# Optimization experiments

Measured on AMD Instinct MI355X. Metric: run time of the kernel, lower is better.

Reference implementation:

```python
import jax, jax.numpy as jnp
import numpy as np
from jax import lax

NUM_HEADS = 8  # init_kwargs: num_heads
TOPK = 7       # hard-coded in DMF.forward


def setup_inputs() -> dict:
    key = jax.random.key(0)
    k1, k2, k3, k4 = jax.random.split(key, 4)
    b, dim, H, W = 8, 384, 128, 128
    x = jax.random.normal(k1, (b, dim, H, W), dtype=jnp.float32)
    qkv_w = jax.random.normal(k2, (dim * 3, dim), dtype=jnp.float32) * 0.05   # 1x1 conv weight
    dw_w = jax.random.normal(k3, (dim * 3, 1, 3, 3), dtype=jnp.float32) * 0.05  # depthwise 3x3
    proj_w = jax.random.normal(k4, (dim, dim), dtype=jnp.float32) * 0.05     # 1x1 conv weight
    temperature = jnp.ones((NUM_HEADS, 1, 1), dtype=jnp.float32)
    return {"x": x, "qkv_w": qkv_w, "dw_w": dw_w, "proj_w": proj_w, "temperature": temperature}


def _l2norm(t, eps=1e-12):
    # matches torch.nn.functional.normalize(dim=-1)
    n = jnp.sqrt(jnp.sum(t * t, axis=-1, keepdims=True))
    return t / jnp.maximum(n, eps)


def reference(x, qkv_w, dw_w, proj_w, temperature):
    b, c, h, w = x.shape
    ch = c // NUM_HEADS  # channels per head

    # 1x1 conv (pointwise) -> depthwise 3x3 conv
    qkv = jnp.einsum('bchw,oc->bohw', x, qkv_w)
    qkv = lax.conv_general_dilated(
        qkv, dw_w, window_strides=(1, 1), padding=[(1, 1), (1, 1)],
        feature_group_count=qkv.shape[1],
        dimension_numbers=('NCHW', 'OIHW', 'NCHW'))
    q, k, v = jnp.split(qkv, 3, axis=1)

    def to_heads(t):  # b (head ch) h w -> b head ch (h w)
        return t.reshape(b, NUM_HEADS, ch, h * w)

    q = _l2norm(to_heads(q))
    k = _l2norm(to_heads(k))
    v = to_heads(v)

    # channel attention: [b, head, ch, ch]
    attn_weight = jnp.einsum('bhcn,bhdn->bhcd', q, k) * temperature

    # top-k sparsify along last dim, then masked softmax
    _, idx = lax.top_k(attn_weight, TOPK)                      # [b,h,ch,TOPK]
    cols = jnp.arange(attn_weight.shape[-1])
    mask = (idx[..., None] == cols).any(axis=-2)               # [b,h,ch,ch] bool
    attn = jnp.where(mask, attn_weight, -jnp.inf)
    attn = jax.nn.softmax(attn, axis=-1)

    out = jnp.einsum('bhcd,bhdn->bhcn', attn, v).reshape(b, c, h, w)
    out = jnp.einsum('bchw,oc->bohw', out, proj_w)
    return out
```

## Files before the change

kernel.cpp:

```cpp
#include <hip/hip_runtime.h>

#define HWN 16384
#define WDIM 128

typedef __bf16 bf16x8 __attribute__((ext_vector_type(8)));
typedef float floatx4 __attribute__((ext_vector_type(4)));

#define LSTR 44

__global__ __launch_bounds__(256, 2) void gemm_mfma3(
    const __bf16* __restrict__ Ah, const __bf16* __restrict__ Al,
    const float* __restrict__ B, float* __restrict__ C,
    int K, long sA, long sB, long sC) {
  __shared__ __bf16 sAh[128 * LSTR], sAl[128 * LSTR], sBh[128 * LSTR], sBl[128 * LSTR];
  const int bz = blockIdx.z;
  Ah += (long)bz * sA;
  Al += (long)bz * sA;
  B += (long)bz * sB;
  C += (long)bz * sC;
  const int tid = threadIdx.x;
  const int n0 = blockIdx.x << 7, m0 = blockIdx.y << 7;
  const int arow = tid >> 1, akq = (tid & 1) << 4;
  const int bn = (tid & 63) << 1;
  const int bkb = (tid >> 6) << 3;
  const int lane = tid & 63, wv = tid >> 6;
  const int mq = (wv & 1) << 6, nq = (wv >> 1) << 6;
  const int fm = lane & 15, fq = lane >> 4;
  floatx4 acc[4][4] = {};
  for (int k0 = 0; k0 < K; k0 += 32) {
    const __bf16* pAh = Ah + (long)(m0 + arow) * K + k0 + akq;
    const __bf16* pAl = Al + (long)(m0 + arow) * K + k0 + akq;
    bf16x8 a0 = *(const bf16x8*)pAh;
    bf16x8 a1 = *(const bf16x8*)(pAh + 8);
    bf16x8 a2 = *(const bf16x8*)pAl;
    bf16x8 a3 = *(const bf16x8*)(pAl + 8);
    const float* pB = B + (long)(k0 + bkb) * HWN + n0 + bn;
    float2 v[8];
#pragma unroll
    for (int r = 0; r < 8; ++r) v[r] = *(const float2*)(pB + (long)r * HWN);
    bf16x8 bh0, bh1, bl0, bl1;
#pragma unroll
    for (int r = 0; r < 8; ++r) {
      float vx = v[r].x, vy = v[r].y;
      __bf16 hx = (__bf16)vx, hy = (__bf16)vy;
      bh0[r] = hx;
      bh1[r] = hy;
      bl0[r] = (__bf16)(vx - (float)hx);
      bl1[r] = (__bf16)(vy - (float)hy);
    }
    __syncthreads();
    *(bf16x8*)&sAh[arow * LSTR + akq] = a0;
    *(bf16x8*)&sAh[arow * LSTR + akq + 8] = a1;
    *(bf16x8*)&sAl[arow * LSTR + akq] = a2;
    *(bf16x8*)&sAl[arow * LSTR + akq + 8] = a3;
    *(bf16x8*)&sBh[bn * LSTR + bkb] = bh0;
    *(bf16x8*)&sBh[(bn + 1) * LSTR + bkb] = bh1;
    *(bf16x8*)&sBl[bn * LSTR + bkb] = bl0;
    *(bf16x8*)&sBl[(bn + 1) * LSTR + bkb] = bl1;
    __syncthreads();
    bf16x8 fAh[4], fAl[4];
#pragma unroll
    for (int i = 0; i < 4; ++i) {
      fAh[i] = *(const bf16x8*)&sAh[(mq + i * 16 + fm) * LSTR + fq * 8];
      fAl[i] = *(const bf16x8*)&sAl[(mq + i * 16 + fm) * LSTR + fq * 8];
    }
#pragma unroll
    for (int j = 0; j < 4; ++j) {
      bf16x8 bh = *(const bf16x8*)&sBh[(nq + j * 16 + fm) * LSTR + fq * 8];
      bf16x8 bl = *(const bf16x8*)&sBl[(nq + j * 16 + fm) * LSTR + fq * 8];
#pragma unroll
      for (int i = 0; i < 4; ++i) {
        acc[i][j] = __builtin_amdgcn_mfma_f32_16x16x32_bf16(fAh[i], bh, acc[i][j], 0, 0, 0);
        acc[i][j] = __builtin_amdgcn_mfma_f32_16x16x32_bf16(fAl[i], bh, acc[i][j], 0, 0, 0);
        acc[i][j] = __builtin_amdgcn_mfma_f32_16x16x32_bf16(fAh[i], bl, acc[i][j], 0, 0, 0);
      }
    }
  }
#pragma unroll
  for (int i = 0; i < 4; ++i)
#pragma unroll
    for (int j = 0; j < 4; ++j) {
      const int col = n0 + nq + j * 16 + fm;
#pragma unroll
      for (int r = 0; r < 4; ++r) {
        const int row = m0 + mq + i * 16 + fq * 4 + r;
        C[(long)row * HWN + col] = acc[i][j][r];
      }
    }
}

__global__ __launch_bounds__(256) void split_w(
    const float* __restrict__ w, __bf16* __restrict__ hi, __bf16* __restrict__ lo, int n) {
  int i = blockIdx.x * 256 + threadIdx.x;
  if (i < n) {
    float v = w[i];
    __bf16 h = (__bf16)v;
    hi[i] = h;
    lo[i] = (__bf16)(v - (float)h);
  }
}

__global__ __launch_bounds__(256) void dw_all2(
    const float* __restrict__ qkv1, const float* __restrict__ dww,
    float* __restrict__ dwout, float* __restrict__ qs, float* __restrict__ ks, int b0) {
  const int tid = threadIdx.x;
  const int ch = blockIdx.x;
  const int bz = blockIdx.y;
  const int xg = tid & 31;
  const int rg = tid >> 5;
  const float4* P = (const float4*)(qkv1 + ((long)bz * 1152 + ch) * HWN);
  float4* O = (float4*)(dwout + ((long)bz * 1152 + ch) * HWN);
  const float* wp = dww + (long)ch * 9;
  const float w00 = wp[0], w01 = wp[1], w02 = wp[2];
  const float w10 = wp[3], w11 = wp[4], w12 = wp[5];
  const float w20 = wp[6], w21 = wp[7], w22 = wp[8];
  const int y0 = rg << 4;

  float e[3][6];
#define LOADROW(Y, E)                                   \
  {                                                     \
    float4 v = make_float4(0.f, 0.f, 0.f, 0.f);         \
    int yy = (Y);                                       \
    if (yy >= 0 && yy < WDIM) v = P[yy * 32 + xg];      \
    float lft = __shfl_up(v.w, 1, 64);                  \
    float rgt = __shfl_down(v.x, 1, 64);                \
    (E)[0] = (xg == 0) ? 0.f : lft;                     \
    (E)[1] = v.x;                                       \
    (E)[2] = v.y;                                       \
    (E)[3] = v.z;                                       \
    (E)[4] = v.w;                                       \
    (E)[5] = (xg == 31) ? 0.f : rgt;                    \
  }

  LOADROW(y0 - 1, e[0]);
  LOADROW(y0, e[1]);
  float sq = 0.f;
#pragma unroll
  for (int i = 0; i < 16; ++i) {
    LOADROW(y0 + i + 1, e[(i + 2) % 3]);
    const float* t = e[i % 3];
    const float* m = e[(i + 1) % 3];
    const float* btm = e[(i + 2) % 3];
    float oarr[4];
#pragma unroll
    for (int j = 0; j < 4; ++j) {
      oarr[j] = w00 * t[j] + w01 * t[j + 1] + w02 * t[j + 2]
              + w10 * m[j] + w11 * m[j + 1] + w12 * m[j + 2]
              + w20 * btm[j] + w21 * btm[j + 1] + w22 * btm[j + 2];
      sq += oarr[j] * oarr[j];
    }
    O[(y0 + i) * 32 + xg] = make_float4(oarr[0], oarr[1], oarr[2], oarr[3]);
  }
#undef LOADROW

  if (ch < 768) {
#pragma unroll
    for (int off = 32; off >= 1; off >>= 1) sq += __shfl_down(sq, off, 64);
    if ((tid & 63) == 0) {
      int b = b0 + bz;
      if (ch < 384)
        atomicAdd(qs + b * 384 + ch, sq);
      else
        atomicAdd(ks + b * 384 + (ch - 384), sq);
    }
  }
}

#define GPAD 132
__global__ __launch_bounds__(256) void gram256(
    const float* __restrict__ dwout, float* __restrict__ gram, int b0) {
  __shared__ float qt[48 * GPAD];
  __shared__ float kt[48 * GPAD];
  const int tid = threadIdx.x;
  const int kc = blockIdx.x;
  const int h = blockIdx.y;
  const int bz = blockIdx.z;
  const float* Q = dwout + ((long)bz * 1152 + h * 48) * HWN;
  const float* K = Q + 384L * HWN;
  const int c0 = (tid & 15) * 3;
  const int d0 = (tid >> 4) * 3;
  float g[3][3] = {};
  for (int p0 = kc * 512; p0 < kc * 512 + 512; p0 += 128) {
    __syncthreads();
#pragma unroll
    for (int i = tid; i < 1536; i += 256) {
      int r = i >> 5, x4 = (i & 31) << 2;
      *(float4*)&qt[r * GPAD + x4] = *(const float4*)(Q + (long)r * HWN + p0 + x4);
      *(float4*)&kt[r * GPAD + x4] = *(const float4*)(K + (long)r * HWN + p0 + x4);
    }
    __syncthreads();
#pragma unroll 4
    for (int p = 0; p < 128; p += 4) {
      float4 qv[3], kv[3];
#pragma unroll
      for (int i = 0; i < 3; ++i) qv[i] = *(const float4*)&qt[(c0 + i) * GPAD + p];
#pragma unroll
      for (int j = 0; j < 3; ++j) kv[j] = *(const float4*)&kt[(d0 + j) * GPAD + p];
#pragma unroll
      for (int i = 0; i < 3; ++i)
#pragma unroll
        for (int j = 0; j < 3; ++j)
          g[i][j] += qv[i].x * kv[j].x + qv[i].y * kv[j].y + qv[i].z * kv[j].z +
                     qv[i].w * kv[j].w;
    }
  }
  float* gb = gram + (long)((b0 + bz) * 8 + h) * 2304;
#pragma unroll
  for (int i = 0; i < 3; ++i)
#pragma unroll
    for (int j = 0; j < 3; ++j) atomicAdd(gb + (c0 + i) * 48 + (d0 + j), g[i][j]);
}

__global__ __launch_bounds__(64) void topk_softmax(
    const float* __restrict__ gram, const float* __restrict__ qs, const float* __restrict__ ks,
    const float* __restrict__ temp, float* __restrict__ attn, int b0) {
  const int z = blockIdx.x;
  const int b = b0 + (z >> 3), h = z & 7;
  __shared__ float kn[48];
  const int tid = threadIdx.x;
  if (tid < 48) kn[tid] = fmaxf(sqrtf(ks[b * 384 + h * 48 + tid]), 1e-12f);
  __syncthreads();
  if (tid >= 48) return;
  const int c = tid;
  float qn = fmaxf(sqrtf(qs[b * 384 + h * 48 + c]), 1e-12f);
  float tv = temp[h];
  const float* gr = gram + (long)(b * 8 + h) * 2304 + c * 48;
  float s[48];
#pragma unroll
  for (int d = 0; d < 48; ++d) s[d] = gr[d] / (qn * kn[d]) * tv;
  unsigned long long sel = 0ull;
  float m0 = 0.f;
  for (int it = 0; it < 7; ++it) {
    float mx = -3.0e38f;
    int mi = 0;
#pragma unroll
    for (int d = 0; d < 48; ++d) {
      bool taken = (sel >> d) & 1ull;
      if (!taken && s[d] > mx) { mx = s[d]; mi = d; }
    }
    sel |= (1ull << mi);
    if (it == 0) m0 = mx;
  }
  float sum = 0.f;
  float e[48];
#pragma unroll
  for (int d = 0; d < 48; ++d) {
    bool t = (sel >> d) & 1ull;
    float ev = t ? expf(s[d] - m0) : 0.f;
    e[d] = ev;
    sum += ev;
  }
  float inv = 1.f / sum;
  float* ar = attn + (long)(b * 8 + h) * 2304 + c * 48;
#pragma unroll
  for (int d = 0; d < 48; ++d) ar[d] = e[d] * inv;
}

__global__ __launch_bounds__(256) void build_M(
    const float* __restrict__ attn, const float* __restrict__ pw,
    __bf16* __restrict__ Mh, __bf16* __restrict__ Ml, int b0) {
  const int b = b0 + blockIdx.x;
  const int h = blockIdx.y;
  __shared__ float at[48][49];
  const int tid = threadIdx.x;
  for (int i = tid; i < 2304; i += 256) at[i / 48][i % 48] = attn[(long)(b * 8 + h) * 2304 + i];
  __syncthreads();
  for (int idx = tid; idx < 384 * 48; idx += 256) {
    int o = idx / 48, d = idx % 48;
    const float* pr = pw + (long)o * 384 + h * 48;
    float acc = 0.f;
#pragma unroll
    for (int c = 0; c < 48; ++c) acc += pr[c] * at[c][d];
    long oi = ((long)b * 384 + o) * 384 + h * 48 + d;
    __bf16 hh = (__bf16)acc;
    Mh[oi] = hh;
    Ml[oi] = (__bf16)(acc - (float)hh);
  }
}

extern "C" void kernel_launch(void* const* d_in, const int* in_sizes, int n_in,
                              void* d_out, int out_size, void* d_ws, size_t ws_size,
                              hipStream_t stream) {
  const float* x = (const float*)d_in[0];
  const float* qkv_w = (const float*)d_in[1];
  const float* dw_w = (const float*)d_in[2];
  const float* proj_w = (const float*)d_in[3];
  const float* temp = (const float*)d_in[4];
  float* out = (float*)d_out;
  float* ws = (float*)d_ws;

  float* gram = ws;
  float* qs = gram + 147456;
  float* ks = qs + 3072;
  float* attn = ks + 3072;
  __bf16* Wh = (__bf16*)(attn + 147456);
  __bf16* Wl = Wh + 442368;
  __bf16* Mh = Wl + 442368;
  __bf16* Ml = Mh + 1179648;
  float* qkv1 = (float*)(Ml + 1179648);
  const long SMALLS = 1333248L;
  const long PERB = 37748736L;
  long wsf = (long)(ws_size / 4);
  int nb = (int)((wsf - SMALLS) / PERB);
  if (nb < 1) nb = 1;
  if (nb > 8) nb = 8;
  float* dwout = qkv1 + (long)nb * 18874368L;

  hipMemsetAsync(gram, 0, (147456 + 3072 + 3072) * sizeof(float), stream);
  split_w<<<dim3((442368 + 255) / 256), 256, 0, stream>>>(qkv_w, Wh, Wl, 442368);

  for (int b0 = 0; b0 < 8; b0 += nb) {
    int nbc = (8 - b0 < nb) ? (8 - b0) : nb;
    gemm_mfma3<<<dim3(128, 9, nbc), 256, 0, stream>>>(
        Wh, Wl, x + (long)b0 * 6291456L, qkv1, 384, 0L, 6291456L, 18874368L);
    dw_all2<<<dim3(1152, nbc), 256, 0, stream>>>(qkv1, dw_w, dwout, qs, ks, b0);
    gram256<<<dim3(32, 8, nbc), 256, 0, stream>>>(dwout, gram, b0);
    topk_softmax<<<dim3(nbc * 8), 64, 0, stream>>>(gram, qs, ks, temp, attn, b0);
    build_M<<<dim3(nbc, 8), 256, 0, stream>>>(attn, proj_w, Mh, Ml, b0);
    gemm_mfma3<<<dim3(128, 3, nbc), 256, 0, stream>>>(
        Mh + (long)b0 * 147456L, Ml + (long)b0 * 147456L, dwout + 768L * HWN,
        out + (long)b0 * 6291456L, 384, 147456L, 18874368L, 6291456L);
  }
}
```

Baseline: 1.402 ms.

## Rewrite split-bf16 GEMM with double-buffered LDS, direct global-to-LDS loads, 128x256 tiles

Replaces the 128x128 single-buffered GEMM with a 512-thread 128x256 tile kernel. The A operand is loaded directly into LDS through global_load_lds, and the B operand is prefetched one K-step ahead in registers and split into bf16 hi/lo before being stored to a second LDS buffer. Manual waitcnt, barriers, sched_barrier and setprio are used to overlap the next tile's loads with the MFMA work. This aims to hide global-load latency and the B conversion, at the cost of more LDS and register pressure and more fragile hand-written synchronisation.

```diff
diff --git a/kernel.cpp b/kernel.cpp
--- a/kernel.cpp
+++ b/kernel.cpp
@@ -6,38 +6,47 @@
 typedef __bf16 bf16x8 __attribute__((ext_vector_type(8)));
 typedef float floatx4 __attribute__((ext_vector_type(4)));
 
-#define LSTR 44
-
-__global__ __launch_bounds__(256, 2) void gemm_mfma3(
+#define BLSTR 44
+
+__device__ __forceinline__ void gload16(const void* g, void* l) {
+  __builtin_amdgcn_global_load_lds(
+      (const __attribute__((address_space(1))) unsigned*)g,
+      (__attribute__((address_space(3))) unsigned*)l, 16, 0, 0);
+}
+
+__global__ __launch_bounds__(512, 2) void gemm8p(
     const __bf16* __restrict__ Ah, const __bf16* __restrict__ Al,
     const float* __restrict__ B, float* __restrict__ C,
     int K, long sA, long sB, long sC) {
-  __shared__ __bf16 sAh[128 * LSTR], sAl[128 * LSTR], sBh[128 * LSTR], sBl[128 * LSTR];
+  __shared__ __bf16 sAh[2][128 * 32], sAl[2][128 * 32];
+  __shared__ __bf16 sBh[2][256 * BLSTR], sBl[2][256 * BLSTR];
   const int bz = blockIdx.z;
   Ah += (long)bz * sA;
   Al += (long)bz * sA;
   B += (long)bz * sB;
   C += (long)bz * sC;
   const int tid = threadIdx.x;
-  const int n0 = blockIdx.x << 7, m0 = blockIdx.y << 7;
-  const int arow = tid >> 1, akq = (tid & 1) << 4;
-  const int bn = (tid & 63) << 1;
-  const int bkb = (tid >> 6) << 3;
+  const int n0 = blockIdx.x << 8, m0 = blockIdx.y << 7;
+  const int ar = tid >> 2, ac = (tid & 3) << 3;
+  const int bpx = (tid & 127) << 1, bkb = (tid >> 7) << 3;
   const int lane = tid & 63, wv = tid >> 6;
   const int mq = (wv & 1) << 6, nq = (wv >> 1) << 6;
   const int fm = lane & 15, fq = lane >> 4;
   floatx4 acc[4][4] = {};
-  for (int k0 = 0; k0 < K; k0 += 32) {
-    const __bf16* pAh = Ah + (long)(m0 + arow) * K + k0 + akq;
-    const __bf16* pAl = Al + (long)(m0 + arow) * K + k0 + akq;
-    bf16x8 a0 = *(const bf16x8*)pAh;
-    bf16x8 a1 = *(const bf16x8*)(pAh + 8);
-    bf16x8 a2 = *(const bf16x8*)pAl;
-    bf16x8 a3 = *(const bf16x8*)(pAl + 8);
-    const float* pB = B + (long)(k0 + bkb) * HWN + n0 + bn;
-    float2 v[8];
+  const int T = K >> 5;
+  float2 v[8];
+  const __bf16* pAh = Ah + (long)(m0 + ar) * K + ac;
+  const __bf16* pAl = Al + (long)(m0 + ar) * K + ac;
+  const int aoff = ar * 32 + ac;
+
+  {
+    const float* pB = B + (long)bkb * HWN + n0 + bpx;
 #pragma unroll
     for (int r = 0; r < 8; ++r) v[r] = *(const float2*)(pB + (long)r * HWN);
+  }
+  gload16(pAh, &sAh[0][aoff]);
+  gload16(pAl, &sAl[0][aoff]);
+  {
     bf16x8 bh0, bh1, bl0, bl1;
 #pragma unroll
     for (int r = 0; r < 8; ++r) {
@@ -48,33 +57,82 @@
       bl0[r] = (__bf16)(vx - (float)hx);
       bl1[r] = (__bf16)(vy - (float)hy);
     }
-    __syncthreads();
-    *(bf16x8*)&sAh[arow * LSTR + akq] = a0;
-    *(bf16x8*)&sAh[arow * LSTR + akq + 8] = a1;
-    *(bf16x8*)&sAl[arow * LSTR + akq] = a2;
-    *(bf16x8*)&sAl[arow * LSTR + akq + 8] = a3;
-    *(bf16x8*)&sBh[bn * LSTR + bkb] = bh0;
-    *(bf16x8*)&sBh[(bn + 1) * LSTR + bkb] = bh1;
-    *(bf16x8*)&sBl[bn * LSTR + bkb] = bl0;
-    *(bf16x8*)&sBl[(bn + 1) * LSTR + bkb] = bl1;
-    __syncthreads();
+    *(bf16x8*)&sBh[0][bpx * BLSTR + bkb] = bh0;
+    *(bf16x8*)&sBh[0][(bpx + 1) * BLSTR + bkb] = bh1;
+    *(bf16x8*)&sBl[0][bpx * BLSTR + bkb] = bl0;
+    *(bf16x8*)&sBl[0][(bpx + 1) * BLSTR + bkb] = bl1;
+  }
+  if (T > 1) {
+    const float* pB = B + (long)(32 + bkb) * HWN + n0 + bpx;
+#pragma unroll
+    for (int r = 0; r < 8; ++r) v[r] = *(const float2*)(pB + (long)r * HWN);
+    asm volatile("s_waitcnt vmcnt(8) lgkmcnt(0)" ::: "memory");
+  } else {
+    asm volatile("s_waitcnt vmcnt(0) lgkmcnt(0)" ::: "memory");
+  }
+  __builtin_amdgcn_s_barrier();
+
+  int cur = 0;
+  for (int t = 0; t < T; ++t) {
+    if (t + 1 < T) {
+      gload16(pAh + (long)(t + 1) * 32, &sAh[cur ^ 1][aoff]);
+      gload16(pAl + (long)(t + 1) * 32, &sAl[cur ^ 1][aoff]);
+    }
+    asm volatile("" ::: "memory");
     bf16x8 fAh[4], fAl[4];
 #pragma unroll
     for (int i = 0; i < 4; ++i) {
-      fAh[i] = *(const bf16x8*)&sAh[(mq + i * 16 + fm) * LSTR + fq * 8];
-      fAl[i] = *(const bf16x8*)&sAl[(mq + i * 16 + fm) * LSTR + fq * 8];
-    }
+      fAh[i] = *(const bf16x8*)&sAh[cur][(mq + i * 16 + fm) * 32 + fq * 8];
+      fAl[i] = *(const bf16x8*)&sAl[cur][(mq + i * 16 + fm) * 32 + fq * 8];
+    }
+    bf16x8 bh[4], bl[4];
+    bh[0] = *(const bf16x8*)&sBh[cur][(nq + fm) * BLSTR + fq * 8];
+    bl[0] = *(const bf16x8*)&sBl[cur][(nq + fm) * BLSTR + fq * 8];
 #pragma unroll
     for (int j = 0; j < 4; ++j) {
-      bf16x8 bh = *(const bf16x8*)&sBh[(nq + j * 16 + fm) * LSTR + fq * 8];
-      bf16x8 bl = *(const bf16x8*)&sBl[(nq + j * 16 + fm) * LSTR + fq * 8];
+      if (j) {
+        __builtin_amdgcn_s_barrier();
+        __builtin_amdgcn_sched_barrier(0);
+      }
+      if (j < 3) {
+        bh[j + 1] = *(const bf16x8*)&sBh[cur][(nq + (j + 1) * 16 + fm) * BLSTR + fq * 8];
+        bl[j + 1] = *(const bf16x8*)&sBl[cur][(nq + (j + 1) * 16 + fm) * BLSTR + fq * 8];
+      }
+      __builtin_amdgcn_s_setprio(1);
 #pragma unroll
       for (int i = 0; i < 4; ++i) {
-        acc[i][j] = __builtin_amdgcn_mfma_f32_16x16x32_bf16(fAh[i], bh, acc[i][j], 0, 0, 0);
-        acc[i][j] = __builtin_amdgcn_mfma_f32_16x16x32_bf16(fAl[i], bh, acc[i][j], 0, 0, 0);
-        acc[i][j] = __builtin_amdgcn_mfma_f32_16x16x32_bf16(fAh[i], bl, acc[i][j], 0, 0, 0);
-      }
-    }
+        acc[i][j] = __builtin_amdgcn_mfma_f32_16x16x32_bf16(fAh[i], bh[j], acc[i][j], 0, 0, 0);
+        acc[i][j] = __builtin_amdgcn_mfma_f32_16x16x32_bf16(fAl[i], bh[j], acc[i][j], 0, 0, 0);
+        acc[i][j] = __builtin_amdgcn_mfma_f32_16x16x32_bf16(fAh[i], bl[j], acc[i][j], 0, 0, 0);
+      }
+      __builtin_amdgcn_s_setprio(0);
+    }
+    if (t + 1 < T) {
+      bf16x8 bh0, bh1, bl0, bl1;
+#pragma unroll
+      for (int r = 0; r < 8; ++r) {
+        float vx = v[r].x, vy = v[r].y;
+        __bf16 hx = (__bf16)vx, hy = (__bf16)vy;
+        bh0[r] = hx;
+        bh1[r] = hy;
+        bl0[r] = (__bf16)(vx - (float)hx);
+        bl1[r] = (__bf16)(vy - (float)hy);
+      }
+      *(bf16x8*)&sBh[cur ^ 1][bpx * BLSTR + bkb] = bh0;
+      *(bf16x8*)&sBh[cur ^ 1][(bpx + 1) * BLSTR + bkb] = bh1;
+      *(bf16x8*)&sBl[cur ^ 1][bpx * BLSTR + bkb] = bl0;
+      *(bf16x8*)&sBl[cur ^ 1][(bpx + 1) * BLSTR + bkb] = bl1;
+      if (t + 2 < T) {
+        const float* pB = B + (long)((t + 2) * 32 + bkb) * HWN + n0 + bpx;
+#pragma unroll
+        for (int r = 0; r < 8; ++r) v[r] = *(const float2*)(pB + (long)r * HWN);
+        asm volatile("s_waitcnt vmcnt(8) lgkmcnt(0)" ::: "memory");
+      } else {
+        asm volatile("s_waitcnt vmcnt(0) lgkmcnt(0)" ::: "memory");
+      }
+      __builtin_amdgcn_s_barrier();
+    }
+    cur ^= 1;
   }
 #pragma unroll
   for (int i = 0; i < 4; ++i)
@@ -311,13 +369,13 @@
 
   for (int b0 = 0; b0 < 8; b0 += nb) {
     int nbc = (8 - b0 < nb) ? (8 - b0) : nb;
-    gemm_mfma3<<<dim3(128, 9, nbc), 256, 0, stream>>>(
+    gemm8p<<<dim3(64, 9, nbc), 512, 0, stream>>>(
         Wh, Wl, x + (long)b0 * 6291456L, qkv1, 384, 0L, 6291456L, 18874368L);
     dw_all2<<<dim3(1152, nbc), 256, 0, stream>>>(qkv1, dw_w, dwout, qs, ks, b0);
     gram256<<<dim3(32, 8, nbc), 256, 0, stream>>>(dwout, gram, b0);
     topk_softmax<<<dim3(nbc * 8), 64, 0, stream>>>(gram, qs, ks, temp, attn, b0);
     build_M<<<dim3(nbc, 8), 256, 0, stream>>>(attn, proj_w, Mh, Ml, b0);
-    gemm_mfma3<<<dim3(128, 3, nbc), 256, 0, stream>>>(
+    gemm8p<<<dim3(64, 3, nbc), 512, 0, stream>>>(
         Mh + (long)b0 * 147456L, Ml + (long)b0 * 147456L, dwout + 768L * HWN,
         out + (long)b0 * 6291456L, 384, 147456L, 18874368L, 6291456L);
   }
```

After: 1.616 ms. 1.15x slower.
